# Kernel tuning notes

Measured on AMD Instinct MI355X. Metric: run time of the kernel, lower is better.

## Reference

```python
import jax, jax.numpy as jnp
import numpy as np

K = 3
STRIDE = 1
PAD = K // 2
GN_GROUPS = 32
EPS = 1e-5


def _conv(x, w, b, stride, pad):
    y = jax.lax.conv_general_dilated(
        x, w, window_strides=(stride, stride),
        padding=[(pad, pad), (pad, pad)],
        dimension_numbers=("NCHW", "OIHW", "NCHW"))
    return y + b[None, :, None, None]


def _bilinear_gather(img, ys, xs):
    # img: [B,C,H,W]; ys/xs: [B,P,Ho,Wo] float sampling coords (zero padding outside)
    B, C, H, W = img.shape
    y0 = jnp.floor(ys)
    x0 = jnp.floor(xs)
    y1, x1 = y0 + 1.0, x0 + 1.0
    wy1 = ys - y0  # weight toward y1
    wx1 = xs - x0
    wy0 = 1.0 - wy1
    wx0 = 1.0 - wx1
    img_flat = img.reshape(B, C, H * W)

    def corner(yc, xc, wgt):
        yi = yc.astype(jnp.int32)
        xi = xc.astype(jnp.int32)
        valid = (yi >= 0) & (yi < H) & (xi >= 0) & (xi < W)
        idx = jnp.clip(yi, 0, H - 1) * W + jnp.clip(xi, 0, W - 1)  # [B,P,Ho,Wo]
        Bp, P, Ho, Wo = idx.shape
        idx_f = jnp.broadcast_to(idx.reshape(B, 1, P * Ho * Wo), (B, C, P * Ho * Wo))
        vals = jnp.take_along_axis(img_flat, idx_f, axis=2).reshape(B, C, P, Ho, Wo)
        w_eff = jnp.where(valid, wgt, 0.0)[:, None]  # [B,1,P,Ho,Wo]
        return vals * w_eff

    out = (corner(y0, x0, wy0 * wx0) + corner(y0, x1, wy0 * wx1)
           + corner(y1, x0, wy1 * wx0) + corner(y1, x1, wy1 * wx1))
    return out  # [B,C,P,Ho,Wo]


def _deform_conv_gn_relu(x, w_off, b_off, w, b, gamma, beta):
    B, C_in, H, W = x.shape
    C_out = w.shape[0]
    P = K * K
    # offset-predicting conv: [B, 2*P, Ho, Wo], channel order (dy0,dx0,dy1,dx1,...)
    off = _conv(x, w_off, b_off, STRIDE, PAD)
    Ho, Wo = off.shape[2], off.shape[3]
    off = off.reshape(B, P, 2, Ho, Wo)
    dy, dx = off[:, :, 0], off[:, :, 1]  # [B,P,Ho,Wo]
    ky, kx = jnp.meshgrid(jnp.arange(K, dtype=x.dtype), jnp.arange(K, dtype=x.dtype), indexing="ij")
    ky, kx = ky.reshape(P), kx.reshape(P)
    base_y = (jnp.arange(Ho, dtype=x.dtype) * STRIDE - PAD)
    base_x = (jnp.arange(Wo, dtype=x.dtype) * STRIDE - PAD)
    ys = base_y[None, None, :, None] + ky[None, :, None, None] + dy
    xs = base_x[None, None, None, :] + kx[None, :, None, None] + dx
    cols = _bilinear_gather(x, ys, xs)  # [B,C_in,P,Ho,Wo]
    y = jnp.einsum("bcphw,ocp->bohw", cols, w.reshape(C_out, C_in, P)) + b[None, :, None, None]
    # GroupNorm(32, C_out)
    G = GN_GROUPS
    yg = y.reshape(B, G, (C_out // G) * Ho * Wo)
    mu = yg.mean(axis=2, keepdims=True)
    var = yg.var(axis=2, keepdims=True)
    yn = ((yg - mu) * jax.lax.rsqrt(var + EPS)).reshape(B, C_out, Ho, Wo)
    yn = yn * gamma[None, :, None, None] + beta[None, :, None, None]
    return jax.nn.relu(yn)


def setup_inputs() -> dict:
    key = jax.random.key(0)
    ks = jax.random.split(key, 7)
    B, C_in, C_out, H, W = 4, 256, 256, 64, 64
    P = K * K
    fan = C_in * P
    x = jax.random.normal(ks[0], (B, C_in, H, W), dtype=jnp.float32)
    w_off = jax.random.normal(ks[1], (2 * P, C_in, K, K), dtype=jnp.float32) * 0.01
    b_off = jnp.zeros((2 * P,), dtype=jnp.float32)
    w = jax.random.normal(ks[2], (C_out, C_in, K, K), dtype=jnp.float32) / np.sqrt(fan)
    b = jax.random.normal(ks[3], (C_out,), dtype=jnp.float32) * 0.01
    gamma = jnp.ones((C_out,), dtype=jnp.float32)
    beta = jnp.zeros((C_out,), dtype=jnp.float32)
    return {"x": x, "w_off": w_off, "b_off": b_off, "w": w, "b": b, "gamma": gamma, "beta": beta}


def reference(x, w_off, b_off, w, b, gamma, beta):
    return _deform_conv_gn_relu(x, w_off, b_off, w, b, gamma, beta)
```

## Files before the change

### kernel.cpp

```cpp
#include <hip/hip_runtime.h>
#include <hip/hip_bf16.h>

using bf16 = __hip_bfloat16;
typedef __attribute__((ext_vector_type(4))) float f32x4;
typedef __attribute__((ext_vector_type(2))) float f32x2;
typedef __attribute__((ext_vector_type(8))) __bf16 bf16x8;
typedef __attribute__((ext_vector_type(4))) __bf16 bf16x4;

#define CIN 256
#define COUT 256
#define HW 4096
#define NB 4
#define NTOT 16384
#define KDIM 2304

__global__ __launch_bounds__(256) void k_transpose(const float* __restrict__ x,
                                                   float* __restrict__ xt) {
  __shared__ float t[32][33];
  int bid = blockIdx.x;
  int ct = bid & 7;
  int hwt = (bid >> 3) & 127;
  int b = bid >> 10;
  int tx = threadIdx.x & 31, ty = threadIdx.x >> 5;
  int c0 = ct * 32, hw0 = hwt * 32;
  const float* xb = x + (size_t)b * CIN * HW;
#pragma unroll
  for (int i = 0; i < 32; i += 8)
    t[ty + i][tx] = xb[(size_t)(c0 + ty + i) * HW + hw0 + tx];
  __syncthreads();
  float* xo = xt + ((size_t)b * HW + hw0) * CIN + c0;
#pragma unroll
  for (int i = 0; i < 32; i += 8)
    xo[(size_t)(ty + i) * CIN + tx] = t[tx][ty + i];
}

__global__ __launch_bounds__(256) void k_prepwt(const float* __restrict__ wof,
                                                float* __restrict__ wt) {
  int i = blockIdx.x * 256 + threadIdx.x;
  if (i >= 18 * CIN * 9) return;
  int oc = i % 18;
  int cp = i / 18;
  int c = cp / 9, p = cp % 9;
  wt[i] = wof[((size_t)oc * CIN + c) * 9 + p];
}

__global__ __launch_bounds__(256) void k_convoff2(const float* __restrict__ x,
                                                  const float* __restrict__ wt,
                                                  float* __restrict__ part) {
  __shared__ float lds[8][6][68];
  int bid = blockIdx.x;
  int chunk = bid & 7;
  int rt = (bid >> 3) & 15;
  int b = bid >> 7;
  int tid = threadIdx.x;
  int wq = tid & 63, r = tid >> 6;
  int h0 = rt * 4;
  int c0 = chunk * 32;

  if (tid < 96) {
    int cl = tid / 12, rem = tid % 12;
    lds[cl][rem >> 1][(rem & 1) ? 66 : 1] = 0.f;
  }

  float acc[18];
#pragma unroll
  for (int o = 0; o < 18; ++o) acc[o] = 0.f;

  int ch = tid >> 5, l32 = tid & 31;
  const float* xb = x + (size_t)b * CIN * HW;

  for (int cs = 0; cs < 32; cs += 8) {
    __syncthreads();
    const float* xp = xb + (size_t)(c0 + cs + ch) * HW;
#pragma unroll
    for (int r6 = 0; r6 < 6; ++r6) {
      int hh = h0 - 1 + r6;
      f32x2 v = {0.f, 0.f};
      if ((unsigned)hh < 64u) v = *(const f32x2*)(xp + hh * 64 + l32 * 2);
      *(f32x2*)&lds[ch][r6][2 + l32 * 2] = v;
    }
    __syncthreads();
#pragma unroll
    for (int cl = 0; cl < 8; ++cl) {
      int c = c0 + cs + cl;
      const float* wc = wt + (size_t)c * 9 * 18;
      float xv[9];
#pragma unroll
      for (int ky = 0; ky < 3; ++ky)
#pragma unroll
        for (int kx = 0; kx < 3; ++kx)
          xv[ky * 3 + kx] = lds[cl][r + ky][1 + wq + kx];
#pragma unroll
      for (int p = 0; p < 9; ++p)
#pragma unroll
        for (int o = 0; o < 18; ++o)
          acc[o] = fmaf(xv[p], wc[p * 18 + o], acc[o]);
    }
  }

  float* pp = part + (size_t)chunk * (NB * 18 * HW) + (size_t)b * 18 * HW +
              (h0 + r) * 64 + wq;
#pragma unroll
  for (int o = 0; o < 18; ++o) pp[(size_t)o * HW] = acc[o];
}

__global__ __launch_bounds__(256) void k_offreduce(const float* __restrict__ part,
                                                   const float* __restrict__ boff,
                                                   float* __restrict__ off) {
  int i = blockIdx.x * 256 + threadIdx.x;
  int e0 = i * 4;
  int oc = (e0 >> 12) % 18;
  float bo = boff[oc];
  f32x4 s = {bo, bo, bo, bo};
#pragma unroll
  for (int c = 0; c < 8; ++c) s += *(const f32x4*)(part + (size_t)c * (NB * 18 * HW) + e0);
  *(f32x4*)(off + e0) = s;
}

__global__ __launch_bounds__(256) void k_prepw(const float* __restrict__ w,
                                               bf16* __restrict__ A) {
  int i = blockIdx.x * 256 + threadIdx.x;
  int o = i / KDIM, r = i % KDIM;
  int p = r >> 8, c = r & 255;
  A[i] = __float2bfloat16(w[((size_t)o * 256 + c) * 9 + p]);
}

__global__ __launch_bounds__(256) void k_gather(const float* __restrict__ xt,
                                                const float* __restrict__ off,
                                                bf16* __restrict__ colsT) {
  int tid = threadIdx.x;
  int wv = tid >> 6, l = tid & 63;
  int n = blockIdx.x * 4 + wv;
  int hw = n & 4095;
  int b = n >> 12;
  int h = hw >> 6, wq = hw & 63;
  const float* xtb = xt + (size_t)b * HW * CIN + l * 4;
  const float* offb = off + (size_t)b * 18 * HW + hw;
  bf16* outp = colsT + (size_t)n * KDIM + l * 4;
#pragma unroll
  for (int p = 0; p < 9; ++p) {
    float dy = offb[(size_t)(2 * p) * HW];
    float dx = offb[(size_t)(2 * p + 1) * HW];
    float ysf = (float)(h - 1 + p / 3) + dy;
    float xsf = (float)(wq - 1 + p % 3) + dx;
    float y0f = floorf(ysf), x0f = floorf(xsf);
    float wy1 = ysf - y0f, wx1 = xsf - x0f;
    float wy0 = 1.f - wy1, wx0 = 1.f - wx1;
    int y0 = (int)y0f, x0 = (int)x0f;
    int y1 = y0 + 1, x1 = x0 + 1;
    float w00 = wy0 * wx0, w01 = wy0 * wx1, w10 = wy1 * wx0, w11 = wy1 * wx1;
    bool vy0 = (unsigned)y0 < 64u, vy1 = (unsigned)y1 < 64u;
    bool vx0 = (unsigned)x0 < 64u, vx1 = (unsigned)x1 < 64u;
    w00 = (vy0 && vx0) ? w00 : 0.f;
    w01 = (vy0 && vx1) ? w01 : 0.f;
    w10 = (vy1 && vx0) ? w10 : 0.f;
    w11 = (vy1 && vx1) ? w11 : 0.f;
    int y0c = min(max(y0, 0), 63), y1c = min(max(y1, 0), 63);
    int x0c = min(max(x0, 0), 63), x1c = min(max(x1, 0), 63);
    f32x4 v00 = *(const f32x4*)(xtb + (size_t)(y0c * 64 + x0c) * CIN);
    f32x4 v01 = *(const f32x4*)(xtb + (size_t)(y0c * 64 + x1c) * CIN);
    f32x4 v10 = *(const f32x4*)(xtb + (size_t)(y1c * 64 + x0c) * CIN);
    f32x4 v11 = *(const f32x4*)(xtb + (size_t)(y1c * 64 + x1c) * CIN);
    f32x4 v;
#pragma unroll
    for (int k = 0; k < 4; ++k)
      v[k] = w00 * v00[k] + w01 * v01[k] + w10 * v10[k] + w11 * v11[k];
    bf16x4 o;
#pragma unroll
    for (int k = 0; k < 4; ++k) o[k] = (__bf16)v[k];
    *(bf16x4*)(outp + p * 256) = o;
  }
}

__global__ __launch_bounds__(256) void k_gemm(const bf16* __restrict__ A,
                                              const bf16* __restrict__ Bt,
                                              const float* __restrict__ bias,
                                              float* __restrict__ Y,
                                              float* __restrict__ gsum,
                                              float* __restrict__ gsq) {
  __shared__ bf16 As[3][128 * 64];
  __shared__ bf16 Bs[3][64 * 64];
  int bid = blockIdx.x;
  int swz = (bid & 7) * 64 + (bid >> 3);
  int mt = swz & 1, nt = swz >> 1;
  int m0 = mt * 128, n0 = nt * 64;
  int tid = threadIdx.x;
  int lane = tid & 63;
  int wave = tid >> 6;
  int wr = (wave >> 1) * 64, wc = (wave & 1) * 32;
  f32x4 acc[4][2];
#pragma unroll
  for (int i = 0; i < 4; ++i)
#pragma unroll
    for (int j = 0; j < 2; ++j) acc[i][j] = (f32x4){0.f, 0.f, 0.f, 0.f};

  int srow = tid >> 3;
  int skdst = (tid & 7) * 8;
  int sksrc = ((tid & 7) ^ ((tid >> 3) & 7)) * 8;
  auto stage = [&](int buf, int kt) {
    int k0 = kt * 64;
#pragma unroll
    for (int ps = 0; ps < 4; ++ps) {
      int r = srow + ps * 32;
      __builtin_amdgcn_global_load_lds(
          (const __attribute__((address_space(1))) void*)(A + (size_t)(m0 + r) * KDIM + k0 + sksrc),
          (__attribute__((address_space(3))) void*)(&As[buf][r * 64 + skdst]), 16, 0, 0);
    }
#pragma unroll
    for (int ps = 0; ps < 2; ++ps) {
      int r = srow + ps * 32;
      __builtin_amdgcn_global_load_lds(
          (const __attribute__((address_space(1))) void*)(Bt + (size_t)(n0 + r) * KDIM + k0 + sksrc),
          (__attribute__((address_space(3))) void*)(&Bs[buf][r * 64 + skdst]), 16, 0, 0);
    }
  };

  int rl = lane & 15;
  int kb = (lane >> 4) * 8;
  int xorv = (rl & 7) * 8;

  constexpr int NT = KDIM / 64;
  stage(0, 0);
  stage(1, 1);

  auto kstep = [&](int kt, int cur, int stg, bool dostage, bool last) {
    if (last) asm volatile("s_waitcnt vmcnt(0)" ::: "memory");
    else      asm volatile("s_waitcnt vmcnt(6)" ::: "memory");
    __builtin_amdgcn_s_barrier();
    if (dostage) stage(stg, kt + 2);
    const bf16* as = As[cur];
    const bf16* bs = Bs[cur];
#pragma unroll
    for (int kh = 0; kh < 2; ++kh) {
      int kc = (kh * 32 + kb) ^ xorv;
      bf16x8 af[4], bfr[2];
#pragma unroll
      for (int i = 0; i < 4; ++i)
        af[i] = *(const bf16x8*)(as + (wr + i * 16 + rl) * 64 + kc);
#pragma unroll
      for (int j = 0; j < 2; ++j)
        bfr[j] = *(const bf16x8*)(bs + (wc + j * 16 + rl) * 64 + kc);
#pragma unroll
      for (int i = 0; i < 4; ++i)
#pragma unroll
        for (int j = 0; j < 2; ++j)
          acc[i][j] = __builtin_amdgcn_mfma_f32_16x16x32_bf16(af[i], bfr[j], acc[i][j], 0, 0, 0);
    }
  };

  for (int kt = 0; kt < NT - 3; kt += 3) {
    kstep(kt + 0, 0, 2, true, false);
    kstep(kt + 1, 1, 0, true, false);
    kstep(kt + 2, 2, 1, true, false);
  }
  kstep(NT - 3, 0, 2, true, false);
  kstep(NT - 2, 1, 0, false, false);
  kstep(NT - 1, 2, 0, false, true);

  int cl = lane & 15, rg = (lane >> 4) * 4;
  int b = n0 >> 12;
#pragma unroll
  for (int i = 0; i < 4; ++i) {
    int obase = m0 + wr + i * 16;
    int ob = obase + rg;
    float s = 0.f, s2 = 0.f;
#pragma unroll
    for (int j = 0; j < 2; ++j) {
      int nn = n0 + wc + j * 16 + cl;
#pragma unroll
      for (int r = 0; r < 4; ++r) {
        float yv = acc[i][j][r] + bias[ob + r];
        Y[(size_t)(ob + r) * NTOT + nn] = yv;
        s += yv;
        s2 = fmaf(yv, yv, s2);
      }
    }
#pragma unroll
    for (int mk = 1; mk <= 16; mk <<= 1) {
      s += __shfl_xor(s, mk);
      s2 += __shfl_xor(s2, mk);
    }
    if ((lane & 31) == 0) {
      int g = (obase >> 3) + (lane >> 5);
      atomicAdd(&gsum[b * 32 + g], s);
      atomicAdd(&gsq[b * 32 + g], s2);
    }
  }
}

__global__ __launch_bounds__(256) void k_apply(const float* __restrict__ Y,
                                               const float* __restrict__ gsum,
                                               const float* __restrict__ gsq,
                                               const float* __restrict__ gamma,
                                               const float* __restrict__ beta,
                                               float* __restrict__ out) {
  int i = blockIdx.x * 256 + threadIdx.x;
  int hw4 = i & 1023;
  int o = (i >> 10) & 255;
  int b = i >> 18;
  int g = o >> 3;
  float mu = gsum[b * 32 + g] * (1.f / 32768.f);
  float var = gsq[b * 32 + g] * (1.f / 32768.f) - mu * mu;
  float rs = rsqrtf(var + 1e-5f);
  float s = rs * gamma[o];
  float t = beta[o] - mu * s;
  f32x4 v = *(const f32x4*)(Y + (size_t)o * NTOT + b * HW + hw4 * 4);
  f32x4 r;
#pragma unroll
  for (int k = 0; k < 4; ++k) r[k] = fmaxf(v[k] * s + t, 0.f);
  *(f32x4*)(out + (size_t)i * 4) = r;
}

extern "C" void kernel_launch(void* const* d_in, const int* in_sizes, int n_in,
                              void* d_out, int out_size, void* d_ws, size_t ws_size,
                              hipStream_t stream) {
  const float* x = (const float*)d_in[0];
  const float* w_off = (const float*)d_in[1];
  const float* b_off = (const float*)d_in[2];
  const float* w = (const float*)d_in[3];
  const float* bias = (const float*)d_in[4];
  const float* gamma = (const float*)d_in[5];
  const float* beta = (const float*)d_in[6];
  float* out = (float*)d_out;
  char* ws = (char*)d_ws;

  float* xt = (float*)(ws);
  float* offb = (float*)(ws + 16777216);
  bf16* Abf = (bf16*)(ws + 16777216 + 1179648);
  bf16* colsT = (bf16*)(ws + 16777216 + 2 * 1179648);
  float* Y = (float*)(ws + 16777216 + 2 * 1179648 + 75497472);
  float* gsum = (float*)(ws + 2 * 16777216 + 2 * 1179648 + 75497472);
  float* gsq = gsum + 128;

  float* wt = (float*)colsT;
  float* part = (float*)((char*)colsT + 262144);

  hipMemsetAsync(gsum, 0, 2 * 128 * sizeof(float), stream);
  k_transpose<<<4096, 256, 0, stream>>>(x, xt);
  k_prepwt<<<162, 256, 0, stream>>>(w_off, wt);
  k_convoff2<<<512, 256, 0, stream>>>(x, wt, part);
  k_offreduce<<<288, 256, 0, stream>>>(part, b_off, offb);
  k_prepw<<<2304, 256, 0, stream>>>(w, Abf);
  k_gather<<<4096, 256, 0, stream>>>(xt, offb, colsT);
  k_gemm<<<512, 256, 0, stream>>>(Abf, colsT, bias, Y, gsum, gsq);
  k_apply<<<4096, 256, 0, stream>>>(Y, gsum, gsq, gamma, beta, out);
}
```

Measured before the change: 142.8 us.

## Fuse deformable bilinear gather into GEMM B-tile staging

After: 144.0 us. No clear change (+0.8%).

```diff
diff --git a/kernel.cpp b/kernel.cpp
--- a/kernel.cpp
+++ b/kernel.cpp
@@ -125,69 +125,24 @@
   A[i] = __float2bfloat16(w[((size_t)o * 256 + c) * 9 + p]);
 }
 
-__global__ __launch_bounds__(256) void k_gather(const float* __restrict__ xt,
-                                                const float* __restrict__ off,
-                                                bf16* __restrict__ colsT) {
-  int tid = threadIdx.x;
-  int wv = tid >> 6, l = tid & 63;
-  int n = blockIdx.x * 4 + wv;
-  int hw = n & 4095;
-  int b = n >> 12;
-  int h = hw >> 6, wq = hw & 63;
-  const float* xtb = xt + (size_t)b * HW * CIN + l * 4;
-  const float* offb = off + (size_t)b * 18 * HW + hw;
-  bf16* outp = colsT + (size_t)n * KDIM + l * 4;
-#pragma unroll
-  for (int p = 0; p < 9; ++p) {
-    float dy = offb[(size_t)(2 * p) * HW];
-    float dx = offb[(size_t)(2 * p + 1) * HW];
-    float ysf = (float)(h - 1 + p / 3) + dy;
-    float xsf = (float)(wq - 1 + p % 3) + dx;
-    float y0f = floorf(ysf), x0f = floorf(xsf);
-    float wy1 = ysf - y0f, wx1 = xsf - x0f;
-    float wy0 = 1.f - wy1, wx0 = 1.f - wx1;
-    int y0 = (int)y0f, x0 = (int)x0f;
-    int y1 = y0 + 1, x1 = x0 + 1;
-    float w00 = wy0 * wx0, w01 = wy0 * wx1, w10 = wy1 * wx0, w11 = wy1 * wx1;
-    bool vy0 = (unsigned)y0 < 64u, vy1 = (unsigned)y1 < 64u;
-    bool vx0 = (unsigned)x0 < 64u, vx1 = (unsigned)x1 < 64u;
-    w00 = (vy0 && vx0) ? w00 : 0.f;
-    w01 = (vy0 && vx1) ? w01 : 0.f;
-    w10 = (vy1 && vx0) ? w10 : 0.f;
-    w11 = (vy1 && vx1) ? w11 : 0.f;
-    int y0c = min(max(y0, 0), 63), y1c = min(max(y1, 0), 63);
-    int x0c = min(max(x0, 0), 63), x1c = min(max(x1, 0), 63);
-    f32x4 v00 = *(const f32x4*)(xtb + (size_t)(y0c * 64 + x0c) * CIN);
-    f32x4 v01 = *(const f32x4*)(xtb + (size_t)(y0c * 64 + x1c) * CIN);
-    f32x4 v10 = *(const f32x4*)(xtb + (size_t)(y1c * 64 + x0c) * CIN);
-    f32x4 v11 = *(const f32x4*)(xtb + (size_t)(y1c * 64 + x1c) * CIN);
-    f32x4 v;
-#pragma unroll
-    for (int k = 0; k < 4; ++k)
-      v[k] = w00 * v00[k] + w01 * v01[k] + w10 * v10[k] + w11 * v11[k];
-    bf16x4 o;
-#pragma unroll
-    for (int k = 0; k < 4; ++k) o[k] = (__bf16)v[k];
-    *(bf16x4*)(outp + p * 256) = o;
-  }
-}
-
-__global__ __launch_bounds__(256) void k_gemm(const bf16* __restrict__ A,
-                                              const bf16* __restrict__ Bt,
-                                              const float* __restrict__ bias,
-                                              float* __restrict__ Y,
-                                              float* __restrict__ gsum,
-                                              float* __restrict__ gsq) {
-  __shared__ bf16 As[3][128 * 64];
-  __shared__ bf16 Bs[3][64 * 64];
+struct GS {
+  f32x4 v00, v01, v10, v11;
+  float w00, w01, w10, w11;
+};
+
+__global__ __launch_bounds__(256) void k_gemm_fused(
+    const bf16* __restrict__ A, const float* __restrict__ xt,
+    const float* __restrict__ off, const float* __restrict__ bias,
+    float* __restrict__ Y, float* __restrict__ gsum, float* __restrict__ gsq) {
+  __shared__ bf16 As[2][256 * 64];
+  __shared__ bf16 Bs[2][32 * 64];
   int bid = blockIdx.x;
   int swz = (bid & 7) * 64 + (bid >> 3);
-  int mt = swz & 1, nt = swz >> 1;
-  int m0 = mt * 128, n0 = nt * 64;
+  int n0 = swz * 32;
   int tid = threadIdx.x;
   int lane = tid & 63;
   int wave = tid >> 6;
-  int wr = (wave >> 1) * 64, wc = (wave & 1) * 32;
+  int wr = wave * 64;
   f32x4 acc[4][2];
 #pragma unroll
   for (int i = 0; i < 4; ++i)
@@ -197,37 +152,95 @@
   int srow = tid >> 3;
   int skdst = (tid & 7) * 8;
   int sksrc = ((tid & 7) ^ ((tid >> 3) & 7)) * 8;
-  auto stage = [&](int buf, int kt) {
+  auto stageA = [&](int buf, int kt) {
     int k0 = kt * 64;
 #pragma unroll
-    for (int ps = 0; ps < 4; ++ps) {
+    for (int ps = 0; ps < 8; ++ps) {
       int r = srow + ps * 32;
       __builtin_amdgcn_global_load_lds(
-          (const __attribute__((address_space(1))) void*)(A + (size_t)(m0 + r) * KDIM + k0 + sksrc),
+          (const __attribute__((address_space(1))) void*)(A + (size_t)r * KDIM + k0 + sksrc),
           (__attribute__((address_space(3))) void*)(&As[buf][r * 64 + skdst]), 16, 0, 0);
     }
-#pragma unroll
-    for (int ps = 0; ps < 2; ++ps) {
-      int r = srow + ps * 32;
-      __builtin_amdgcn_global_load_lds(
-          (const __attribute__((address_space(1))) void*)(Bt + (size_t)(n0 + r) * KDIM + k0 + sksrc),
-          (__attribute__((address_space(3))) void*)(&Bs[buf][r * 64 + skdst]), 16, 0, 0);
-    }
   };
+
+  int b = n0 >> 12;
+  const float* xtb = xt + (size_t)b * HW * CIN;
+  const float* offb = off + (size_t)b * 18 * HW;
+  int l16 = lane & 15, grp = lane >> 4;
+  int nl0 = wave * 8 + grp;
+
+  auto stageB_load = [&](GS (&gs)[2], int kt) {
+    int p = kt >> 2;
+    int c0s = (kt & 3) * 64;
+    int py = p / 3 - 1, px = p % 3 - 1;
+    const float* base = xtb + c0s + l16 * 4;
+#pragma unroll
+    for (int pass = 0; pass < 2; ++pass) {
+      int nl = nl0 + pass * 4;
+      int hw = (n0 + nl) & 4095;
+      int h = hw >> 6, wq = hw & 63;
+      float dy = offb[(size_t)(2 * p) * HW + hw];
+      float dx = offb[(size_t)(2 * p + 1) * HW + hw];
+      float ysf = (float)(h + py) + dy;
+      float xsf = (float)(wq + px) + dx;
+      float y0f = floorf(ysf), x0f = floorf(xsf);
+      float wy1 = ysf - y0f, wx1 = xsf - x0f;
+      float wy0 = 1.f - wy1, wx0 = 1.f - wx1;
+      int y0 = (int)y0f, x0 = (int)x0f;
+      int y1 = y0 + 1, x1 = x0 + 1;
+      float w00 = wy0 * wx0, w01 = wy0 * wx1, w10 = wy1 * wx0, w11 = wy1 * wx1;
+      bool vy0 = (unsigned)y0 < 64u, vy1 = (unsigned)y1 < 64u;
+      bool vx0 = (unsigned)x0 < 64u, vx1 = (unsigned)x1 < 64u;
+      gs[pass].w00 = (vy0 && vx0) ? w00 : 0.f;
+      gs[pass].w01 = (vy0 && vx1) ? w01 : 0.f;
+      gs[pass].w10 = (vy1 && vx0) ? w10 : 0.f;
+      gs[pass].w11 = (vy1 && vx1) ? w11 : 0.f;
+      int y0c = min(max(y0, 0), 63), y1c = min(max(y1, 0), 63);
+      int x0c = min(max(x0, 0), 63), x1c = min(max(x1, 0), 63);
+      gs[pass].v00 = *(const f32x4*)(base + (size_t)(y0c * 64 + x0c) * CIN);
+      gs[pass].v01 = *(const f32x4*)(base + (size_t)(y0c * 64 + x1c) * CIN);
+      gs[pass].v10 = *(const f32x4*)(base + (size_t)(y1c * 64 + x0c) * CIN);
+      gs[pass].v11 = *(const f32x4*)(base + (size_t)(y1c * 64 + x1c) * CIN);
+    }
+  };
+
+  auto stageB_write = [&](GS (&gs)[2], int buf) {
+#pragma unroll
+    for (int pass = 0; pass < 2; ++pass) {
+      int nl = nl0 + pass * 4;
+      f32x4 v;
+#pragma unroll
+      for (int k = 0; k < 4; ++k)
+        v[k] = gs[pass].w00 * gs[pass].v00[k] + gs[pass].w01 * gs[pass].v01[k] +
+               gs[pass].w10 * gs[pass].v10[k] + gs[pass].w11 * gs[pass].v11[k];
+      bf16x4 o;
+#pragma unroll
+      for (int k = 0; k < 4; ++k) o[k] = (__bf16)v[k];
+      int el = (l16 * 4) ^ ((nl & 7) * 8);
+      *(bf16x4*)(&Bs[buf][nl * 64 + el]) = o;
+    }
+  };
+
+  constexpr int NT = KDIM / 64;
+  stageA(0, 0);
+  {
+    GS g0[2];
+    stageB_load(g0, 0);
+    stageB_write(g0, 0);
+  }
 
   int rl = lane & 15;
   int kb = (lane >> 4) * 8;
   int xorv = (rl & 7) * 8;
 
-  constexpr int NT = KDIM / 64;
-  stage(0, 0);
-  stage(1, 1);
-
-  auto kstep = [&](int kt, int cur, int stg, bool dostage, bool last) {
-    if (last) asm volatile("s_waitcnt vmcnt(0)" ::: "memory");
-    else      asm volatile("s_waitcnt vmcnt(6)" ::: "memory");
-    __builtin_amdgcn_s_barrier();
-    if (dostage) stage(stg, kt + 2);
+  for (int kt = 0; kt < NT; ++kt) {
+    int cur = kt & 1;
+    __syncthreads();
+    GS gs[2];
+    if (kt + 1 < NT) {
+      stageA(cur ^ 1, kt + 1);
+      stageB_load(gs, kt + 1);
+    }
     const bf16* as = As[cur];
     const bf16* bs = Bs[cur];
 #pragma unroll
@@ -239,34 +252,25 @@
         af[i] = *(const bf16x8*)(as + (wr + i * 16 + rl) * 64 + kc);
 #pragma unroll
       for (int j = 0; j < 2; ++j)
-        bfr[j] = *(const bf16x8*)(bs + (wc + j * 16 + rl) * 64 + kc);
+        bfr[j] = *(const bf16x8*)(bs + (j * 16 + rl) * 64 + kc);
 #pragma unroll
       for (int i = 0; i < 4; ++i)
 #pragma unroll
         for (int j = 0; j < 2; ++j)
           acc[i][j] = __builtin_amdgcn_mfma_f32_16x16x32_bf16(af[i], bfr[j], acc[i][j], 0, 0, 0);
     }
-  };
-
-  for (int kt = 0; kt < NT - 3; kt += 3) {
-    kstep(kt + 0, 0, 2, true, false);
-    kstep(kt + 1, 1, 0, true, false);
-    kstep(kt + 2, 2, 1, true, false);
-  }
-  kstep(NT - 3, 0, 2, true, false);
-  kstep(NT - 2, 1, 0, false, false);
-  kstep(NT - 1, 2, 0, false, true);
+    if (kt + 1 < NT) stageB_write(gs, cur ^ 1);
+  }
 
   int cl = lane & 15, rg = (lane >> 4) * 4;
-  int b = n0 >> 12;
 #pragma unroll
   for (int i = 0; i < 4; ++i) {
-    int obase = m0 + wr + i * 16;
+    int obase = wr + i * 16;
     int ob = obase + rg;
     float s = 0.f, s2 = 0.f;
 #pragma unroll
     for (int j = 0; j < 2; ++j) {
-      int nn = n0 + wc + j * 16 + cl;
+      int nn = n0 + j * 16 + cl;
 #pragma unroll
       for (int r = 0; r < 4; ++r) {
         float yv = acc[i][j][r] + bias[ob + r];
@@ -327,13 +331,13 @@
   float* xt = (float*)(ws);
   float* offb = (float*)(ws + 16777216);
   bf16* Abf = (bf16*)(ws + 16777216 + 1179648);
-  bf16* colsT = (bf16*)(ws + 16777216 + 2 * 1179648);
+  char* scratch = ws + 16777216 + 2 * 1179648;
   float* Y = (float*)(ws + 16777216 + 2 * 1179648 + 75497472);
   float* gsum = (float*)(ws + 2 * 16777216 + 2 * 1179648 + 75497472);
   float* gsq = gsum + 128;
 
-  float* wt = (float*)colsT;
-  float* part = (float*)((char*)colsT + 262144);
+  float* wt = (float*)scratch;
+  float* part = (float*)(scratch + 262144);
 
   hipMemsetAsync(gsum, 0, 2 * 128 * sizeof(float), stream);
   k_transpose<<<4096, 256, 0, stream>>>(x, xt);
@@ -341,7 +345,6 @@
   k_convoff2<<<512, 256, 0, stream>>>(x, wt, part);
   k_offreduce<<<288, 256, 0, stream>>>(part, b_off, offb);
   k_prepw<<<2304, 256, 0, stream>>>(w, Abf);
-  k_gather<<<4096, 256, 0, stream>>>(xt, offb, colsT);
-  k_gemm<<<512, 256, 0, stream>>>(Abf, colsT, bias, Y, gsum, gsq);
+  k_gemm_fused<<<512, 256, 0, stream>>>(Abf, xt, offb, bias, Y, gsum, gsq);
   k_apply<<<4096, 256, 0, stream>>>(Y, gsum, gsq, gamma, beta, out);
 }
```
